# Performance work log

Hardware: AMD Instinct MI355X
Metric: run time of the kernel (lower is better)

Reference implementation:

```python
import jax, jax.numpy as jnp
import numpy as np

B, V, N, S, F, H, K, STEPS = 8, 3, 400, 1200, 16, 32, 10, 12
ALPHA_FUSE = 0.8
NEG = -9e15


def setup_inputs() -> dict:
    key = jax.random.key(0)
    ks = jax.random.split(key, 16)
    g = lambda i, shape, s=0.1: jax.random.normal(ks[i], shape, jnp.float32) * s
    return {
        "feat": jax.random.normal(ks[0], (B, S, F), jnp.float32),
        "adj": jax.random.bernoulli(ks[1], 0.05, (B, V, S, S)).astype(jnp.float32),
        "dis_lab": jax.random.uniform(ks[2], (B, K), dtype=jnp.float32),
        "W_gat": g(3, (V, F, H), 0.3),
        "a_gat": g(4, (V, 2 * H, 1), 0.3),
        "qkv_W": g(5, (H, 3 * H)),
        "qkv_b": jnp.zeros((3 * H,), jnp.float32),
        "o_W": g(6, (H, H)),
        "o_b": jnp.zeros((H,), jnp.float32),
        "fus_W": g(7, (H, H)),
        "fus_b": jnp.zeros((H,), jnp.float32),
        "att1_W": g(8, (2 * H, H)),
        "att1_b": jnp.zeros((H,), jnp.float32),
        "att2_W": g(9, (H, 1)),
        "att2_b": jnp.zeros((1,), jnp.float32),
        "gru_Wih": g(10, (H, 3 * H)),
        "gru_Whh": g(11, (H, 3 * H)),
        "gru_bih": jnp.zeros((3 * H,), jnp.float32),
        "gru_bhh": jnp.zeros((3 * H,), jnp.float32),
        "out_W": g(12, (H, 1)),
        "out_b": jnp.zeros((1,), jnp.float32),
    }


def _forward(feat, adj, dis_lab, W_gat, a_gat, qkv_W, qkv_b, o_W, o_b,
             fus_W, fus_b, att1_W, att1_b, att2_W, att2_b,
             gru_Wih, gru_Whh, gru_bih, gru_bhh, out_W, out_b):
    # ---- per-view GAT (masked softmax over dense adjacency) ----
    Wh = jnp.einsum('bsf,vfh->bvsh', feat, W_gat)            # [B,V,S,H]
    a1, a2 = a_gat[:, :H, 0], a_gat[:, H:, 0]
    e = (jnp.einsum('bvsh,vh->bvs', Wh, a1)[..., :, None]
         + jnp.einsum('bvsh,vh->bvs', Wh, a2)[..., None, :])  # [B,V,S,S]
    e = jax.nn.leaky_relu(e, 0.2)
    e = jnp.where(adj > 0, e, NEG)
    att = jax.nn.softmax(e, axis=-1)
    hid = jax.nn.elu(jnp.einsum('bvst,bvth->bvsh', att, Wh))  # [B,V,S,H]
    # ---- cross-view self-attention fusion (single head) ----
    x = hid.reshape(B, V * S, H)
    q, k, v = jnp.split(x @ qkv_W + qkv_b, 3, axis=-1)
    logits = jnp.einsum('bld,bmd->blm', q, k) / jnp.sqrt(jnp.float32(H))
    sa = jnp.einsum('blm,bmd->bld', jax.nn.softmax(logits, axis=-1), v)
    sa = sa @ o_W + o_b
    hfuse = (ALPHA_FUSE * sa + (1.0 - ALPHA_FUSE) * x).reshape(B, V, S, H)
    gate = jax.nn.sigmoid(hfuse @ fus_W + fus_b)
    fusion = jnp.sum(gate * hfuse, axis=1)[:, 2 * N:, :]      # [B,N,H]
    # ---- attention over label stations ----
    label = fusion[:, :K, :]                                  # [B,K,H]
    unlabel = fusion[:, K, :]                                 # [B,H]
    cat = jnp.concatenate([label, jnp.broadcast_to(unlabel[:, None, :], label.shape)], axis=-1)
    s = jax.nn.relu(cat @ att1_W + att1_b) @ att2_W + att2_b  # [B,K,1]
    score = jax.nn.softmax(s[..., 0] * dis_lab, axis=1)
    ctx = jnp.einsum('bk,bkh->bh', score, label)
    # ---- GRU decoder (feed hidden state back as next input) ----
    def gru_cell(xt, h):
        gi = xt @ gru_Wih + gru_bih
        gh = h @ gru_Whh + gru_bhh
        ir, iz, inn = jnp.split(gi, 3, axis=-1)
        hr, hz, hn = jnp.split(gh, 3, axis=-1)
        r = jax.nn.sigmoid(ir + hr)
        z = jax.nn.sigmoid(iz + hz)
        n = jnp.tanh(inn + r * hn)
        return (1.0 - z) * n + z * h
    def step(carry, _):
        xt, h = carry
        h2 = gru_cell(xt, h)
        out = h2 @ out_W + out_b
        return (h2, h2), out[:, 0]
    _, outs = jax.lax.scan(step, (ctx, unlabel), None, length=STEPS)
    return outs.T  # [B, STEPS]


def reference(feat, adj, dis_lab, W_gat, a_gat, qkv_W, qkv_b, o_W, o_b,
              fus_W, fus_b, att1_W, att1_b, att2_W, att2_b,
              gru_Wih, gru_Whh, gru_bih, gru_bhh, out_W, out_b):
    return _forward(feat, adj, dis_lab, W_gat, a_gat, qkv_W, qkv_b, o_W, o_b,
                    fus_W, fus_b, att1_W, att1_b, att2_W, att2_b,
                    gru_Wih, gru_Whh, gru_bih, gru_bhh, out_W, out_b)
```

## Files before the change

### kernel.cpp

```cpp
#include <hip/hip_runtime.h>
#include <math.h>

#define Bb 8
#define Vv 3
#define Ss 1200
#define Ff 16
#define Hh 32
#define Kk 10
#define STEPS 12
#define ROWS (Bb*Vv*Ss)
#define L (Vv*Ss)
#define KPAD 1216
#define NKB 152
#define MROW 40

typedef __attribute__((ext_vector_type(8))) short bf16x8;
typedef __attribute__((ext_vector_type(4))) float f32x4;
typedef __attribute__((ext_vector_type(4))) unsigned int u32x4;

__device__ __forceinline__ unsigned int pack_hi2(float x0, float x1) {
    return (__float_as_uint(x1) & 0xFFFF0000u) | (__float_as_uint(x0) >> 16);
}
__device__ __forceinline__ unsigned int pack_lo2(float x0, float x1) {
    float h0 = __uint_as_float(__float_as_uint(x0) & 0xFFFF0000u);
    float h1 = __uint_as_float(__float_as_uint(x1) & 0xFFFF0000u);
    return (__float_as_uint(x1 - h1) & 0xFFFF0000u) | (__float_as_uint(x0 - h0) >> 16);
}
__device__ __forceinline__ unsigned int spread4(unsigned int x) {
    x = (x | (x << 12)) & 0x000F000Fu;
    x = (x | (x << 6))  & 0x03030303u;
    x = (x | (x << 3))  & 0x11111111u;
    return x;
}

__global__ __launch_bounds__(256) void gat_wh_k(const float* __restrict__ feat,
                                                const float* __restrict__ W_gat,
                                                const float* __restrict__ a_gat,
                                                float* __restrict__ Wh,
                                                float* __restrict__ fvec,
                                                float* __restrict__ gvec) {
    int blk = blockIdx.x;
    int c = blk % 150;
    int v = (blk / 150) % Vv;
    int b = blk / (150 * Vv);
    int tid = threadIdx.x;
    int r = tid >> 5;
    int h = tid & 31;
    int s = c * 8 + r;

    __shared__ float Wg[16][32];
    __shared__ float fe[8][16];
    for (int i = tid; i < 512; i += 256) Wg[i >> 5][i & 31] = W_gat[v * 512 + i];
    for (int i = tid; i < 128; i += 256) fe[i >> 4][i & 15] = feat[(b * Ss + c * 8) * Ff + i];
    __syncthreads();

    float acc = 0.f;
#pragma unroll
    for (int k = 0; k < 16; ++k) acc += fe[r][k] * Wg[k][h];

    int row = (b * Vv + v) * Ss + s;
    Wh[(size_t)row * Hh + h] = acc;

    float a1 = a_gat[v * 64 + h];
    float a2 = a_gat[v * 64 + 32 + h];
    float pf = acc * a1, pg = acc * a2;
#pragma unroll
    for (int m = 16; m >= 1; m >>= 1) {
        pf += __shfl_xor(pf, m);
        pg += __shfl_xor(pg, m);
    }
    if (h == 0) { fvec[row] = pf; gvec[row] = pg; }
}

__global__ __launch_bounds__(256) void gmax_k(const float* __restrict__ gvec,
                                              float* __restrict__ Gmax) {
    int bv = blockIdx.x;
    int tid = threadIdx.x;
    float m = -3.0e38f;
    for (int t = tid; t < Ss; t += 256) m = fmaxf(m, gvec[bv * Ss + t]);
#pragma unroll
    for (int mm = 32; mm >= 1; mm >>= 1) m = fmaxf(m, __shfl_xor(m, mm));
    __shared__ float red[4];
    if ((tid & 63) == 0) red[tid >> 6] = m;
    __syncthreads();
    if (tid == 0) Gmax[bv] = fmaxf(fmaxf(red[0], red[1]), fmaxf(red[2], red[3]));
}

__global__ __launch_bounds__(256) void wht_k(const float* __restrict__ Wh,
                                             ushort* __restrict__ WhT) {
    int bv = blockIdx.x / 19, t = blockIdx.x % 19;
    int s0 = t * 64;
    int tid = threadIdx.x;
    __shared__ float T[64][33];
    for (int idx = tid; idx < 2048; idx += 256) {
        int r = idx >> 5, h = idx & 31;
        T[r][h] = (s0 + r < Ss) ? Wh[((size_t)bv * Ss + s0 + r) * Hh + h] : 0.f;
    }
    __syncthreads();
    int h = tid >> 3, c = tid & 7;
    int kb = (s0 >> 3) + c;
    unsigned int hb[4], lb[4];
#pragma unroll
    for (int j = 0; j < 4; ++j) {
        float e0 = T[c * 8 + 2 * j][h], e1 = T[c * 8 + 2 * j + 1][h];
        hb[j] = pack_hi2(e0, e1);
        lb[j] = pack_lo2(e0, e1);
    }
    size_t base = (((size_t)bv * NKB + kb) * 2) * 256 + h * 8;
    *(uint4*)(WhT + base)       = make_uint4(hb[0], hb[1], hb[2], hb[3]);
    *(uint4*)(WhT + base + 256) = make_uint4(lb[0], lb[1], lb[2], lb[3]);
}

__global__ __launch_bounds__(256) void adj_pack_k(const float* __restrict__ adj,
                                                  unsigned int* __restrict__ maskb) {
    int gw = (blockIdx.x * 256 + threadIdx.x) >> 6;
    int lane = threadIdx.x & 63;
    for (int row = gw; row < ROWS; row += 5760) {
        const float* ar = adj + (size_t)row * Ss;
        unsigned int* mrow = maskb + (size_t)row * MROW;
#pragma unroll
        for (int c = 0; c < 5; ++c) {
            int base = c * 256 + lane * 4;
            bool v = (base + 3) < Ss;
            float4 a = v ? *(const float4*)(ar + base) : make_float4(0.f, 0.f, 0.f, 0.f);
            unsigned long long b0 = __ballot(v && (a.x > 0.f));
            unsigned long long b1 = __ballot(v && (a.y > 0.f));
            unsigned long long b2 = __ballot(v && (a.z > 0.f));
            unsigned long long b3 = __ballot(v && (a.w > 0.f));
            int nw = (c == 4) ? 6 : 8;
            if (lane < nw) {
                int sh = 8 * lane;
                unsigned int B0 = (unsigned int)(b0 >> sh) & 0xFFu;
                unsigned int B1 = (unsigned int)(b1 >> sh) & 0xFFu;
                unsigned int B2 = (unsigned int)(b2 >> sh) & 0xFFu;
                unsigned int B3 = (unsigned int)(b3 >> sh) & 0xFFu;
                mrow[c * 8 + lane] = spread4(B0) | (spread4(B1) << 1)
                                   | (spread4(B2) << 2) | (spread4(B3) << 3);
            }
        }
        if (lane < 2) mrow[38 + lane] = 0u;
    }
}

__global__ __launch_bounds__(256) void gat_mfma_k(const unsigned int* __restrict__ maskb,
                                                  const ushort* __restrict__ WhT,
                                                  const float* __restrict__ fvec,
                                                  const float* __restrict__ gvec,
                                                  const float* __restrict__ Gmax,
                                                  float* __restrict__ hid,
                                                  float* __restrict__ hsel) {
    int blk = blockIdx.x;
    int bv = blk / 75, tb = blk % 75;
    int wk = threadIdx.x >> 6, lane = threadIdx.x & 63;
    int rowbase = tb * 16;
    int lr = lane & 15, kg = lane >> 4;
    int b = bv / Vv, v = bv - b * Vv;

    int ar = rowbase + lr;
    const float* g_b = gvec + (size_t)bv * Ss;
    float fr = fvec[bv * Ss + ar];
    float M = fr + Gmax[bv];
    float Mr = fmaxf(M, 0.2f * M);

    const unsigned int* mrow = maskb + (size_t)(bv * Ss + ar) * MROW + wk * 10;
    unsigned int mw[10];
#pragma unroll
    for (int i = 0; i < 5; ++i) {
        uint2 t = *(const uint2*)(mrow + 2 * i);
        mw[2 * i] = t.x; mw[2 * i + 1] = t.y;
    }

    f32x4 acc0 = {0.f, 0.f, 0.f, 0.f}, acc1 = {0.f, 0.f, 0.f, 0.f};
    float psum = 0.f;
    const ushort* Wbv = WhT + ((size_t)bv * NKB) * 512;

    int kst = wk * 320;
#pragma unroll
    for (int s = 0; s < 10; ++s) {
        int k0 = kst + s * 32;
        if (k0 < KPAD) {
            int t0 = k0 + kg * 8;
            int kb = t0 >> 3;
            unsigned int mb = (mw[s] >> (kg * 8)) & 0xFFu;

            const ushort* Bp = Wbv + (size_t)kb * 512 + lr * 8;
            bf16x8 bh0 = *(const bf16x8*)(Bp);
            bf16x8 bh1 = *(const bf16x8*)(Bp + 128);
            bf16x8 bl0 = *(const bf16x8*)(Bp + 256);
            bf16x8 bl1 = *(const bf16x8*)(Bp + 384);

            float gv8[8];
            if (t0 + 8 <= Ss) {
                float4 gA = *(const float4*)(g_b + t0);
                float4 gB = *(const float4*)(g_b + t0 + 4);
                gv8[0] = gA.x; gv8[1] = gA.y; gv8[2] = gA.z; gv8[3] = gA.w;
                gv8[4] = gB.x; gv8[5] = gB.y; gv8[6] = gB.z; gv8[7] = gB.w;
            } else {
#pragma unroll
                for (int j = 0; j < 8; ++j) gv8[j] = 0.f;
            }
            float p[8];
#pragma unroll
            for (int j = 0; j < 8; ++j) {
                float e = fr + gv8[j];
                e = fmaxf(e, 0.2f * e);
                float pe = __expf(e - Mr);
                p[j] = ((mb >> j) & 1u) ? pe : 0.f;
                psum += p[j];
            }
            unsigned int hbp[4], lbp[4];
#pragma unroll
            for (int j = 0; j < 4; ++j) {
                hbp[j] = pack_hi2(p[2 * j], p[2 * j + 1]);
                lbp[j] = pack_lo2(p[2 * j], p[2 * j + 1]);
            }
            bf16x8 ah = __builtin_bit_cast(bf16x8, (u32x4){hbp[0], hbp[1], hbp[2], hbp[3]});
            bf16x8 al = __builtin_bit_cast(bf16x8, (u32x4){lbp[0], lbp[1], lbp[2], lbp[3]});
            acc0 = __builtin_amdgcn_mfma_f32_16x16x32_bf16(ah, bh0, acc0, 0, 0, 0);
            acc0 = __builtin_amdgcn_mfma_f32_16x16x32_bf16(ah, bl0, acc0, 0, 0, 0);
            acc0 = __builtin_amdgcn_mfma_f32_16x16x32_bf16(al, bh0, acc0, 0, 0, 0);
            acc1 = __builtin_amdgcn_mfma_f32_16x16x32_bf16(ah, bh1, acc1, 0, 0, 0);
            acc1 = __builtin_amdgcn_mfma_f32_16x16x32_bf16(ah, bl1, acc1, 0, 0, 0);
            acc1 = __builtin_amdgcn_mfma_f32_16x16x32_bf16(al, bh1, acc1, 0, 0, 0);
        }
    }

    psum += __shfl_xor(psum, 16);
    psum += __shfl_xor(psum, 32);

    __shared__ float accS[4][2][16][17];
    __shared__ float psS[4][16];
#pragma unroll
    for (int j = 0; j < 4; ++j) {
        accS[wk][0][kg * 4 + j][lr] = acc0[j];
        accS[wk][1][kg * 4 + j][lr] = acc1[j];
    }
    if (lane < 16) psS[wk][lr] = psum;
    __syncthreads();
    if (threadIdx.x < 16)
        psS[0][threadIdx.x] += psS[1][threadIdx.x] + psS[2][threadIdx.x] + psS[3][threadIdx.x];
    __syncthreads();

    bool qb = (tb == 50);
    for (int idx = threadIdx.x; idx < 512; idx += 256) {
        int r = idx >> 5, col = idx & 31, tt = col >> 4, c = col & 15;
        float a = accS[0][tt][r][c] + accS[1][tt][r][c] + accS[2][tt][r][c] + accS[3][tt][r][c];
        float rr = a / psS[0][r];
        float hv = (rr > 0.f) ? rr : expm1f(rr);
        hid[((size_t)bv * Ss + rowbase + r) * 32 + col] = hv;
        if (qb && r < 11) hsel[(((size_t)b * Vv + v) * 11 + r) * 32 + col] = hv;
    }
}

__global__ __launch_bounds__(256) void attn_q_k(const float* __restrict__ hsel,
                                                const float* __restrict__ qkv_W,
                                                const float* __restrict__ qkv_b,
                                                float* __restrict__ qt,
                                                float* __restrict__ qc) {
    int b = blockIdx.x;
    int tid = threadIdx.x;
    __shared__ float hq[33][33];
    __shared__ float W1[32][33];
    __shared__ float W2[32][33];
    __shared__ float qS[33][33];

    for (int idx = tid; idx < 33 * 32; idx += 256) {
        int q = idx >> 5, i = idx & 31;
        int si = q / 3, v = q - si * 3;
        hq[q][i] = hsel[(((size_t)b * Vv + v) * 11 + si) * 32 + i];
    }
    for (int idx = tid; idx < 1024; idx += 256) {
        int i = idx >> 5, j = idx & 31;
        W1[i][j] = qkv_W[i * 96 + j];
        W2[i][j] = qkv_W[i * 96 + 32 + j];
    }
    __syncthreads();
    for (int idx = tid; idx < 33 * 32; idx += 256) {
        int q = idx >> 5, j = idx & 31;
        float a = qkv_b[j];
#pragma unroll
        for (int i = 0; i < 32; ++i) a += hq[q][i] * W1[i][j];
        qS[q][j] = a;
    }
    __syncthreads();
    for (int idx = tid; idx < 33 * 32; idx += 256) {
        int q = idx >> 5, i = idx & 31;
        float a = 0.f;
#pragma unroll
        for (int j = 0; j < 32; ++j) a += qS[q][j] * W2[i][j];
        qt[(size_t)b * 33 * 32 + q * 32 + i] = a;
    }
    if (tid < 33) {
        float a = 0.f;
        for (int j = 0; j < 32; ++j) a += qS[tid][j] * qkv_b[32 + j];
        qc[b * 33 + tid] = a;
    }
}

#define CH 120
#define NCH 30
#define PREC 34
__global__ __launch_bounds__(256) void attn_part_k(const float* __restrict__ hid,
                                                   const float* __restrict__ qt,
                                                   const float* __restrict__ qc,
                                                   float* __restrict__ part) {
    int blk = blockIdx.x;
    int b = blk / NCH, ch = blk % NCH;
    int k0 = ch * CH;
    int tid = threadIdx.x;
    const float inv = 0.1767766952966369f;

    __shared__ float hC[CH][33];
    __shared__ float qtS[33][33];
    __shared__ float qcS[33];
    __shared__ float lS[33][124];
    __shared__ float mS[33], lsS[33];

    for (int idx = tid; idx < CH * 32; idx += 256) {
        int r = idx >> 5, i = idx & 31;
        hC[r][i] = hid[((size_t)b * L + k0 + r) * 32 + i];
    }
    for (int idx = tid; idx < 33 * 32; idx += 256) {
        int q = idx >> 5, i = idx & 31;
        qtS[q][i] = qt[(size_t)b * 33 * 32 + q * 32 + i];
    }
    if (tid < 33) qcS[tid] = qc[b * 33 + tid];
    __syncthreads();

    for (int idx = tid; idx < 33 * CH; idx += 256) {
        int q = idx / CH, m = idx - q * CH;
        float d = 0.f;
#pragma unroll
        for (int i = 0; i < 32; ++i) d += qtS[q][i] * hC[m][i];
        lS[q][m] = (d + qcS[q]) * inv;
    }
    __syncthreads();

    int q4 = tid >> 2, j4 = tid & 3;
    if (q4 < 33) {
        float m = -3.0e38f;
        for (int k = j4; k < CH; k += 4) m = fmaxf(m, lS[q4][k]);
        m = fmaxf(m, __shfl_xor(m, 1));
        m = fmaxf(m, __shfl_xor(m, 2));
        float ssum = 0.f;
        for (int k = j4; k < CH; k += 4) {
            float p = __expf(lS[q4][k] - m);
            lS[q4][k] = p;
            ssum += p;
        }
        ssum += __shfl_xor(ssum, 1);
        ssum += __shfl_xor(ssum, 2);
        if (j4 == 0) { mS[q4] = m; lsS[q4] = ssum; }
    }
    __syncthreads();

    float* po = part + ((size_t)b * NCH + ch) * (33 * PREC);
    for (int idx = tid; idx < 33 * 32; idx += 256) {
        int q = idx >> 5, hh = idx & 31;
        float a = 0.f;
        for (int k = 0; k < CH; k += 4) {
            float4 p4 = *(const float4*)&lS[q][k];
            a += p4.x * hC[k][hh] + p4.y * hC[k+1][hh] + p4.z * hC[k+2][hh] + p4.w * hC[k+3][hh];
        }
        po[q * PREC + hh] = a;
    }
    if (tid < 33) { po[tid * PREC + 32] = mS[tid]; po[tid * PREC + 33] = lsS[tid]; }
}

__global__ __launch_bounds__(256) void attn_comb_k(const float* __restrict__ part,
                                                   const float* __restrict__ hsel,
                                                   const float* __restrict__ qkv_W,
                                                   const float* __restrict__ qkv_b,
                                                   const float* __restrict__ o_W,
                                                   const float* __restrict__ o_b,
                                                   const float* __restrict__ fus_W,
                                                   const float* __restrict__ fus_b,
                                                   float* __restrict__ hfg) {
    int b = blockIdx.x;
    int tid = threadIdx.x;
    __shared__ float RS[33][NCH];
    __shared__ float LSs[33];
    __shared__ float oS[33][33];
    __shared__ float vS[33][33];
    __shared__ float hfS[33][33];
    const float* pb = part + (size_t)b * NCH * (33 * PREC);

    if (tid < 33) {
        float M = -3.0e38f;
        for (int c = 0; c < NCH; ++c) M = fmaxf(M, pb[c * 33 * PREC + tid * PREC + 32]);
        float Lt = 0.f;
        for (int c = 0; c < NCH; ++c) {
            float w = __expf(pb[c * 33 * PREC + tid * PREC + 32] - M);
            RS[tid][c] = w;
            Lt += w * pb[c * 33 * PREC + tid * PREC + 33];
        }
        LSs[tid] = Lt;
    }
    __syncthreads();

    for (int idx = tid; idx < 33 * 32; idx += 256) {
        int q = idx >> 5, hh = idx & 31;
        float a = 0.f;
        for (int c = 0; c < NCH; ++c) a += RS[q][c] * pb[c * 33 * PREC + q * PREC + hh];
        oS[q][hh] = a / LSs[q];
    }
    __syncthreads();
    for (int idx = tid; idx < 33 * 32; idx += 256) {
        int q = idx >> 5, j = idx & 31;
        float a = qkv_b[64 + j];
#pragma unroll
        for (int i = 0; i < 32; ++i) a += oS[q][i] * qkv_W[i * 96 + 64 + j];
        vS[q][j] = a;
    }
    __syncthreads();
    for (int idx = tid; idx < 33 * 32; idx += 256) {
        int q = idx >> 5, hh = idx & 31;
        int si = q / 3, v = q - si * 3;
        float o = o_b[hh];
#pragma unroll
        for (int i = 0; i < 32; ++i) o += vS[q][i] * o_W[i * 32 + hh];
        float x = hsel[(((size_t)b * Vv + v) * 11 + si) * Hh + hh];
        hfS[q][hh] = 0.8f * o + 0.2f * x;
    }
    __syncthreads();
    for (int idx = tid; idx < 33 * 32; idx += 256) {
        int q = idx >> 5, hh = idx & 31;
        float gacc = fus_b[hh];
#pragma unroll
        for (int i = 0; i < 32; ++i) gacc += hfS[q][i] * fus_W[i * 32 + hh];
        float gate = 1.f / (1.f + __expf(-gacc));
        hfg[(size_t)(b * 33 + q) * 32 + hh] = gate * hfS[q][hh];
    }
}

__global__ __launch_bounds__(64) void head_k(const float* __restrict__ hfg,
                                             const float* __restrict__ dis_lab,
                                             const float* __restrict__ att1_W,
                                             const float* __restrict__ att1_b,
                                             const float* __restrict__ att2_W,
                                             const float* __restrict__ att2_b,
                                             const float* __restrict__ Wih,
                                             const float* __restrict__ Whh,
                                             const float* __restrict__ bih,
                                             const float* __restrict__ bhh,
                                             const float* __restrict__ out_W,
                                             const float* __restrict__ out_b,
                                             float* __restrict__ out) {
    int b = blockIdx.x;
    int tid = threadIdx.x;
    int j = tid & 31, half = tid >> 5;

    __shared__ float lab[11][32];
    __shared__ float a1T[32][68];
    __shared__ float WihT[3][32][36];
    __shared__ float WhhT[3][32][36];
    __shared__ float sc[12];
    __shared__ float xS[32], hS[32];

    for (int i = tid; i < 352; i += 64) {
        int k = i >> 5, hh = i & 31;
        float val = 0.f;
#pragma unroll
        for (int v = 0; v < 3; ++v) val += hfg[(size_t)(b * 33 + k * 3 + v) * 32 + hh];
        lab[k][hh] = val;
    }
    for (int idx = tid; idx < 2048; idx += 64) {
        int i = idx >> 5, jj = idx & 31;
        a1T[jj][i] = att1_W[idx];
    }
    for (int idx = tid; idx < 3072; idx += 64) {
        int i = idx / 96, col = idx - i * 96;
        int g = col >> 5, jj = col & 31;
        WihT[g][jj][i] = Wih[idx];
        WhhT[g][jj][i] = Whh[idx];
    }
    __syncthreads();

    float a2w = att2_W[j];
    float a1b = att1_b[j];
    float a2b = att2_b[0];
#pragma unroll
    for (int kk = 0; kk < 5; ++kk) {
        int k = 2 * kk + half;
        float t1 = a1b;
#pragma unroll
        for (int c = 0; c < 8; ++c) {
            float4 lb4 = *(const float4*)&lab[k][c * 4];
            float4 w4  = *(const float4*)&a1T[j][c * 4];
            t1 += lb4.x * w4.x + lb4.y * w4.y + lb4.z * w4.z + lb4.w * w4.w;
        }
#pragma unroll
        for (int c = 0; c < 8; ++c) {
            float4 lb4 = *(const float4*)&lab[10][c * 4];
            float4 w4  = *(const float4*)&a1T[j][32 + c * 4];
            t1 += lb4.x * w4.x + lb4.y * w4.y + lb4.z * w4.z + lb4.w * w4.w;
        }
        float val = fmaxf(t1, 0.f) * a2w;
#pragma unroll
        for (int mm = 16; mm >= 1; mm >>= 1) val += __shfl_xor(val, mm);
        if (j == 0) sc[k] = (val + a2b) * dis_lab[b * Kk + k];
    }
    __syncthreads();
    if (tid == 0) {
        float mx = sc[0];
        for (int k = 1; k < 10; ++k) mx = fmaxf(mx, sc[k]);
        float sm = 0.f;
        for (int k = 0; k < 10; ++k) { sc[k] = __expf(sc[k] - mx); sm += sc[k]; }
        for (int k = 0; k < 10; ++k) sc[k] /= sm;
    }
    __syncthreads();
    if (tid < 32) {
        float c = 0.f;
        for (int k = 0; k < 10; ++k) c += sc[k] * lab[k][tid];
        xS[tid] = c;
        hS[tid] = lab[10][tid];
    }
    __syncthreads();

    float b_ir = bih[j], b_iz = bih[32 + j], b_in = bih[64 + j];
    float b_hr = bhh[j], b_hz = bhh[32 + j], b_hn = bhh[64 + j];
    float ow = out_W[j], ob = out_b[0];
    int i0 = half * 16;

    for (int t = 0; t < STEPS; ++t) {
        float gi_r = 0.f, gi_z = 0.f, gi_n = 0.f;
        float gh_r = 0.f, gh_z = 0.f, gh_n = 0.f;
#pragma unroll
        for (int c = 0; c < 4; ++c) {
            float4 x4 = *(const float4*)&xS[i0 + c * 4];
            float4 h4 = *(const float4*)&hS[i0 + c * 4];
            float4 wr = *(const float4*)&WihT[0][j][i0 + c * 4];
            float4 wz = *(const float4*)&WihT[1][j][i0 + c * 4];
            float4 wn = *(const float4*)&WihT[2][j][i0 + c * 4];
            float4 ur = *(const float4*)&WhhT[0][j][i0 + c * 4];
            float4 uz = *(const float4*)&WhhT[1][j][i0 + c * 4];
            float4 un = *(const float4*)&WhhT[2][j][i0 + c * 4];
            gi_r += x4.x * wr.x + x4.y * wr.y + x4.z * wr.z + x4.w * wr.w;
            gi_z += x4.x * wz.x + x4.y * wz.y + x4.z * wz.z + x4.w * wz.w;
            gi_n += x4.x * wn.x + x4.y * wn.y + x4.z * wn.z + x4.w * wn.w;
            gh_r += h4.x * ur.x + h4.y * ur.y + h4.z * ur.z + h4.w * ur.w;
            gh_z += h4.x * uz.x + h4.y * uz.y + h4.z * uz.z + h4.w * uz.w;
            gh_n += h4.x * un.x + h4.y * un.y + h4.z * un.z + h4.w * un.w;
        }
        gi_r += __shfl_xor(gi_r, 32); gi_z += __shfl_xor(gi_z, 32); gi_n += __shfl_xor(gi_n, 32);
        gh_r += __shfl_xor(gh_r, 32); gh_z += __shfl_xor(gh_z, 32); gh_n += __shfl_xor(gh_n, 32);

        float hprev = hS[j];
        float r = 1.f / (1.f + __expf(-(gi_r + b_ir + gh_r + b_hr)));
        float z = 1.f / (1.f + __expf(-(gi_z + b_iz + gh_z + b_hz)));
        float n = tanhf(gi_n + b_in + r * (gh_n + b_hn));
        float hnew = (1.f - z) * n + z * hprev;

        float outp = hnew * ow;
#pragma unroll
        for (int mm = 16; mm >= 1; mm >>= 1) outp += __shfl_xor(outp, mm);
        if (tid == 0) out[b * STEPS + t] = outp + ob;
        __syncthreads();
        if (tid < 32) { hS[tid] = hnew; xS[tid] = hnew; }
        __syncthreads();
    }
}

extern "C" void kernel_launch(void* const* d_in, const int* in_sizes, int n_in,
                              void* d_out, int out_size, void* d_ws, size_t ws_size,
                              hipStream_t stream) {
    const float* feat    = (const float*)d_in[0];
    const float* adj     = (const float*)d_in[1];
    const float* dis_lab = (const float*)d_in[2];
    const float* W_gat   = (const float*)d_in[3];
    const float* a_gat   = (const float*)d_in[4];
    const float* qkv_W   = (const float*)d_in[5];
    const float* qkv_b   = (const float*)d_in[6];
    const float* o_W     = (const float*)d_in[7];
    const float* o_b     = (const float*)d_in[8];
    const float* fus_W   = (const float*)d_in[9];
    const float* fus_b   = (const float*)d_in[10];
    const float* att1_W  = (const float*)d_in[11];
    const float* att1_b  = (const float*)d_in[12];
    const float* att2_W  = (const float*)d_in[13];
    const float* att2_b  = (const float*)d_in[14];
    const float* Wih     = (const float*)d_in[15];
    const float* Whh     = (const float*)d_in[16];
    const float* bih     = (const float*)d_in[17];
    const float* bhh     = (const float*)d_in[18];
    const float* out_W   = (const float*)d_in[19];
    const float* out_b   = (const float*)d_in[20];
    float* out = (float*)d_out;

    float* ws = (float*)d_ws;
    float*  Wh     = ws;
    float*  hid    = ws;
    float*  fvec   = ws + 921600;
    float*  gvec   = ws + 950400;
    float*  Gmax   = ws + 979200;
    ushort* WhT    = (ushort*)(ws + 979232);
    float*  part   = ws + 979232;
    float*  hsel   = ws + 1913120;
    float*  hfg    = ws + 1921568;
    float*  qt     = ws + 1930016;
    float*  qc     = ws + 1938464;
    unsigned int* maskb = (unsigned int*)(ws + 1938752);

    adj_pack_k<<<dim3(1440), dim3(256), 0, stream>>>(adj, maskb);
    gat_wh_k<<<dim3(Bb * Vv * 150), dim3(256), 0, stream>>>(feat, W_gat, a_gat, Wh, fvec, gvec);
    gmax_k<<<dim3(Bb * Vv), dim3(256), 0, stream>>>(gvec, Gmax);
    wht_k<<<dim3(Bb * Vv * 19), dim3(256), 0, stream>>>(Wh, WhT);
    gat_mfma_k<<<dim3(Bb * Vv * 75), dim3(256), 0, stream>>>(maskb, WhT,
                                                             fvec, gvec, Gmax, hid, hsel);
    attn_q_k<<<dim3(Bb), dim3(256), 0, stream>>>(hsel, qkv_W, qkv_b, qt, qc);
    attn_part_k<<<dim3(Bb * NCH), dim3(256), 0, stream>>>(hid, qt, qc, part);
    attn_comb_k<<<dim3(Bb), dim3(256), 0, stream>>>(part, hsel, qkv_W, qkv_b,
                                                    o_W, o_b, fus_W, fus_b, hfg);
    head_k<<<dim3(Bb), dim3(64), 0, stream>>>(hfg, dis_lab, att1_W, att1_b, att2_W, att2_b,
                                              Wih, Whh, bih, bhh, out_W, out_b, out);
}
```

Measured before the change: 132.8 us.

## Split GAT K-loop across eight waves and preload all B fragments

The GAT aggregation kernel now runs eight waves per block instead of four. Each wave handles 160 keys over five steps instead of 320 over ten, and the key padding grows to 1280 so the split is even. Each wave loads all of its Wh^T fragments into registers before the exp/MFMA loop, which is meant to hide global-load latency and shorten each wave's serial chain. In exchange it uses more registers, a larger shared-memory reduction, slightly more padded work, and a reshuffled workspace layout.

```diff
diff --git a/kernel.cpp b/kernel.cpp
--- a/kernel.cpp
+++ b/kernel.cpp
@@ -10,8 +10,8 @@
 #define STEPS 12
 #define ROWS (Bb*Vv*Ss)
 #define L (Vv*Ss)
-#define KPAD 1216
-#define NKB 152
+#define KPAD 1280
+#define NKB 160
 #define MROW 40
 
 typedef __attribute__((ext_vector_type(8))) short bf16x8;
@@ -88,7 +88,7 @@
 
 __global__ __launch_bounds__(256) void wht_k(const float* __restrict__ Wh,
                                              ushort* __restrict__ WhT) {
-    int bv = blockIdx.x / 19, t = blockIdx.x % 19;
+    int bv = blockIdx.x / 20, t = blockIdx.x % 20;
     int s0 = t * 64;
     int tid = threadIdx.x;
     __shared__ float T[64][33];
@@ -98,7 +98,7 @@
     }
     __syncthreads();
     int h = tid >> 3, c = tid & 7;
-    int kb = (s0 >> 3) + c;
+    int kb = t * 8 + c;
     unsigned int hb[4], lb[4];
 #pragma unroll
     for (int j = 0; j < 4; ++j) {
@@ -142,7 +142,7 @@
     }
 }
 
-__global__ __launch_bounds__(256) void gat_mfma_k(const unsigned int* __restrict__ maskb,
+__global__ __launch_bounds__(512) void gat_mfma_k(const unsigned int* __restrict__ maskb,
                                                   const ushort* __restrict__ WhT,
                                                   const float* __restrict__ fvec,
                                                   const float* __restrict__ gvec,
@@ -162,74 +162,70 @@
     float M = fr + Gmax[bv];
     float Mr = fmaxf(M, 0.2f * M);
 
-    const unsigned int* mrow = maskb + (size_t)(bv * Ss + ar) * MROW + wk * 10;
-    unsigned int mw[10];
-#pragma unroll
-    for (int i = 0; i < 5; ++i) {
-        uint2 t = *(const uint2*)(mrow + 2 * i);
-        mw[2 * i] = t.x; mw[2 * i + 1] = t.y;
+    const unsigned int* mrow = maskb + (size_t)(bv * Ss + ar) * MROW + wk * 5;
+    unsigned int mw[5];
+#pragma unroll
+    for (int i = 0; i < 5; ++i) mw[i] = mrow[i];
+
+    const ushort* Wbv = WhT + (size_t)bv * NKB * 512;
+    int kst = wk * 160;
+    bf16x8 Bh0[5], Bh1[5], Bl0[5], Bl1[5];
+#pragma unroll
+    for (int s = 0; s < 5; ++s) {
+        int kb = wk * 20 + s * 4 + kg;
+        const ushort* Bp = Wbv + (size_t)kb * 512 + lr * 8;
+        Bh0[s] = *(const bf16x8*)(Bp);
+        Bh1[s] = *(const bf16x8*)(Bp + 128);
+        Bl0[s] = *(const bf16x8*)(Bp + 256);
+        Bl1[s] = *(const bf16x8*)(Bp + 384);
     }
 
     f32x4 acc0 = {0.f, 0.f, 0.f, 0.f}, acc1 = {0.f, 0.f, 0.f, 0.f};
     float psum = 0.f;
-    const ushort* Wbv = WhT + ((size_t)bv * NKB) * 512;
-
-    int kst = wk * 320;
-#pragma unroll
-    for (int s = 0; s < 10; ++s) {
-        int k0 = kst + s * 32;
-        if (k0 < KPAD) {
-            int t0 = k0 + kg * 8;
-            int kb = t0 >> 3;
-            unsigned int mb = (mw[s] >> (kg * 8)) & 0xFFu;
-
-            const ushort* Bp = Wbv + (size_t)kb * 512 + lr * 8;
-            bf16x8 bh0 = *(const bf16x8*)(Bp);
-            bf16x8 bh1 = *(const bf16x8*)(Bp + 128);
-            bf16x8 bl0 = *(const bf16x8*)(Bp + 256);
-            bf16x8 bl1 = *(const bf16x8*)(Bp + 384);
-
-            float gv8[8];
-            if (t0 + 8 <= Ss) {
-                float4 gA = *(const float4*)(g_b + t0);
-                float4 gB = *(const float4*)(g_b + t0 + 4);
-                gv8[0] = gA.x; gv8[1] = gA.y; gv8[2] = gA.z; gv8[3] = gA.w;
-                gv8[4] = gB.x; gv8[5] = gB.y; gv8[6] = gB.z; gv8[7] = gB.w;
-            } else {
-#pragma unroll
-                for (int j = 0; j < 8; ++j) gv8[j] = 0.f;
-            }
-            float p[8];
-#pragma unroll
-            for (int j = 0; j < 8; ++j) {
-                float e = fr + gv8[j];
-                e = fmaxf(e, 0.2f * e);
-                float pe = __expf(e - Mr);
-                p[j] = ((mb >> j) & 1u) ? pe : 0.f;
-                psum += p[j];
-            }
-            unsigned int hbp[4], lbp[4];
-#pragma unroll
-            for (int j = 0; j < 4; ++j) {
-                hbp[j] = pack_hi2(p[2 * j], p[2 * j + 1]);
-                lbp[j] = pack_lo2(p[2 * j], p[2 * j + 1]);
-            }
-            bf16x8 ah = __builtin_bit_cast(bf16x8, (u32x4){hbp[0], hbp[1], hbp[2], hbp[3]});
-            bf16x8 al = __builtin_bit_cast(bf16x8, (u32x4){lbp[0], lbp[1], lbp[2], lbp[3]});
-            acc0 = __builtin_amdgcn_mfma_f32_16x16x32_bf16(ah, bh0, acc0, 0, 0, 0);
-            acc0 = __builtin_amdgcn_mfma_f32_16x16x32_bf16(ah, bl0, acc0, 0, 0, 0);
-            acc0 = __builtin_amdgcn_mfma_f32_16x16x32_bf16(al, bh0, acc0, 0, 0, 0);
-            acc1 = __builtin_amdgcn_mfma_f32_16x16x32_bf16(ah, bh1, acc1, 0, 0, 0);
-            acc1 = __builtin_amdgcn_mfma_f32_16x16x32_bf16(ah, bl1, acc1, 0, 0, 0);
-            acc1 = __builtin_amdgcn_mfma_f32_16x16x32_bf16(al, bh1, acc1, 0, 0, 0);
-        }
+#pragma unroll
+    for (int s = 0; s < 5; ++s) {
+        int t0 = kst + s * 32 + kg * 8;
+        unsigned int mb = (mw[s] >> (kg * 8)) & 0xFFu;
+        float gv8[8];
+        if (t0 + 8 <= Ss) {
+            float4 gA = *(const float4*)(g_b + t0);
+            float4 gB = *(const float4*)(g_b + t0 + 4);
+            gv8[0] = gA.x; gv8[1] = gA.y; gv8[2] = gA.z; gv8[3] = gA.w;
+            gv8[4] = gB.x; gv8[5] = gB.y; gv8[6] = gB.z; gv8[7] = gB.w;
+        } else {
+#pragma unroll
+            for (int j = 0; j < 8; ++j) gv8[j] = 0.f;
+        }
+        float p[8];
+#pragma unroll
+        for (int j = 0; j < 8; ++j) {
+            float e = fr + gv8[j];
+            e = fmaxf(e, 0.2f * e);
+            float pe = __expf(e - Mr);
+            p[j] = ((mb >> j) & 1u) ? pe : 0.f;
+            psum += p[j];
+        }
+        unsigned int hbp[4], lbp[4];
+#pragma unroll
+        for (int j = 0; j < 4; ++j) {
+            hbp[j] = pack_hi2(p[2 * j], p[2 * j + 1]);
+            lbp[j] = pack_lo2(p[2 * j], p[2 * j + 1]);
+        }
+        bf16x8 ah = __builtin_bit_cast(bf16x8, (u32x4){hbp[0], hbp[1], hbp[2], hbp[3]});
+        bf16x8 al = __builtin_bit_cast(bf16x8, (u32x4){lbp[0], lbp[1], lbp[2], lbp[3]});
+        acc0 = __builtin_amdgcn_mfma_f32_16x16x32_bf16(ah, Bh0[s], acc0, 0, 0, 0);
+        acc0 = __builtin_amdgcn_mfma_f32_16x16x32_bf16(ah, Bl0[s], acc0, 0, 0, 0);
+        acc0 = __builtin_amdgcn_mfma_f32_16x16x32_bf16(al, Bh0[s], acc0, 0, 0, 0);
+        acc1 = __builtin_amdgcn_mfma_f32_16x16x32_bf16(ah, Bh1[s], acc1, 0, 0, 0);
+        acc1 = __builtin_amdgcn_mfma_f32_16x16x32_bf16(ah, Bl1[s], acc1, 0, 0, 0);
+        acc1 = __builtin_amdgcn_mfma_f32_16x16x32_bf16(al, Bh1[s], acc1, 0, 0, 0);
     }
 
     psum += __shfl_xor(psum, 16);
     psum += __shfl_xor(psum, 32);
 
-    __shared__ float accS[4][2][16][17];
-    __shared__ float psS[4][16];
+    __shared__ float accS[8][2][16][17];
+    __shared__ float psS[8][16];
 #pragma unroll
     for (int j = 0; j < 4; ++j) {
         accS[wk][0][kg * 4 + j][lr] = acc0[j];
@@ -237,14 +233,21 @@
     }
     if (lane < 16) psS[wk][lr] = psum;
     __syncthreads();
-    if (threadIdx.x < 16)
-        psS[0][threadIdx.x] += psS[1][threadIdx.x] + psS[2][threadIdx.x] + psS[3][threadIdx.x];
+    if (threadIdx.x < 16) {
+        float t = 0.f;
+#pragma unroll
+        for (int w = 0; w < 8; ++w) t += psS[w][threadIdx.x];
+        psS[0][threadIdx.x] = t;
+    }
     __syncthreads();
 
     bool qb = (tb == 50);
-    for (int idx = threadIdx.x; idx < 512; idx += 256) {
+    {
+        int idx = threadIdx.x;
         int r = idx >> 5, col = idx & 31, tt = col >> 4, c = col & 15;
-        float a = accS[0][tt][r][c] + accS[1][tt][r][c] + accS[2][tt][r][c] + accS[3][tt][r][c];
+        float a = 0.f;
+#pragma unroll
+        for (int w = 0; w < 8; ++w) a += accS[w][tt][r][c];
         float rr = a / psS[0][r];
         float hv = (rr > 0.f) ? rr : expm1f(rr);
         hid[((size_t)bv * Ss + rowbase + r) * 32 + col] = hv;
@@ -595,17 +598,17 @@
     float*  Gmax   = ws + 979200;
     ushort* WhT    = (ushort*)(ws + 979232);
     float*  part   = ws + 979232;
-    float*  hsel   = ws + 1913120;
-    float*  hfg    = ws + 1921568;
-    float*  qt     = ws + 1930016;
-    float*  qc     = ws + 1938464;
-    unsigned int* maskb = (unsigned int*)(ws + 1938752);
+    float*  hsel   = ws + 1962272;
+    float*  hfg    = ws + 1970720;
+    float*  qt     = ws + 1979168;
+    float*  qc     = ws + 1987616;
+    unsigned int* maskb = (unsigned int*)(ws + 1987904);
 
     adj_pack_k<<<dim3(1440), dim3(256), 0, stream>>>(adj, maskb);
     gat_wh_k<<<dim3(Bb * Vv * 150), dim3(256), 0, stream>>>(feat, W_gat, a_gat, Wh, fvec, gvec);
     gmax_k<<<dim3(Bb * Vv), dim3(256), 0, stream>>>(gvec, Gmax);
-    wht_k<<<dim3(Bb * Vv * 19), dim3(256), 0, stream>>>(Wh, WhT);
-    gat_mfma_k<<<dim3(Bb * Vv * 75), dim3(256), 0, stream>>>(maskb, WhT,
+    wht_k<<<dim3(Bb * Vv * 20), dim3(256), 0, stream>>>(Wh, WhT);
+    gat_mfma_k<<<dim3(Bb * Vv * 75), dim3(512), 0, stream>>>(maskb, WhT,
                                                              fvec, gvec, Gmax, hid, hsel);
     attn_q_k<<<dim3(Bb), dim3(256), 0, stream>>>(hsel, qkv_W, qkv_b, qt, qc);
     attn_part_k<<<dim3(Bb * NCH), dim3(256), 0, stream>>>(hid, qt, qc, part);
```

After: 137.5 us. +3.6%, slower.
